# Kernel optimization log

Measured on AMD Instinct MI355X. Metric: run time of the kernel, lower is better.

Reference implementation:

```python
import jax, jax.numpy as jnp
import numpy as np

D = 1024
N_PASSES = 2


def _hadamard(d):
    # Sylvester construction: d must be a power of 2
    H = np.array([[1.0]], dtype=np.float32)
    while H.shape[0] < d:
        H = np.block([[H, H], [H, -H]])
    return H


def setup_inputs() -> dict:
    key = jax.random.key(0)
    kx, ks = jax.random.split(key)
    x = jax.random.normal(kx, (8, 8192, D), dtype=jnp.float32)
    # random +/-1 sign vectors, one per pass
    signs = jnp.where(jax.random.bernoulli(ks, 0.5, (N_PASSES, D)), 1.0, -1.0).astype(jnp.float32)
    h_mat = jnp.asarray(_hadamard(D))  # unnormalized Walsh-Hadamard matrix [D, D]
    return {"x": x, "signs": signs, "h_mat": h_mat}


def reference(x, signs, h_mat):
    # Cascaded SRHT: (sign flip -> WHT -> scale by 1/sqrt(d)) x n_passes
    d = x.shape[-1]
    scale = 1.0 / jnp.sqrt(jnp.asarray(d, dtype=x.dtype))
    out = x
    for i in range(N_PASSES):
        out = (out * signs[i]) @ h_mat * scale
    return out
```

## Files before the change

### kernel.cpp

```cpp
#include <hip/hip_runtime.h>

#define DD 1024

typedef float f32x4 __attribute__((ext_vector_type(4)));

__device__ __forceinline__ void fwht16(float (&v)[16]) {
  #pragma unroll
  for (int h = 1; h < 16; h <<= 1) {
    #pragma unroll
    for (int i = 0; i < 16; ++i) {
      if (!(i & h)) {
        float a = v[i], b = v[i | h];
        v[i]     = a + b;
        v[i | h] = a - b;
      }
    }
  }
}

__device__ __forceinline__ void shfl_stage(float (&v)[16], int mask, int lane) {
  const float sgn = (lane & mask) ? -1.0f : 1.0f;
  #pragma unroll
  for (int j = 0; j < 16; ++j) {
    float o = __shfl_xor(v[j], mask, 64);
    v[j] = fmaf(sgn, v[j], o);
  }
}

__global__ __launch_bounds__(256) void srht_kernel(
    const float* __restrict__ x,
    const float* __restrict__ signs,
    float* __restrict__ out)
{
  __shared__ float lds[4][DD];
  const int lane = threadIdx.x & 63;
  const int wv   = threadIdx.x >> 6;
  const long row = (long)blockIdx.x * 4 + wv;

  const float* __restrict__ xr = x + row * DD;
  float* __restrict__ orow     = out + row * DD;
  const float* __restrict__ s0 = signs;
  const float* __restrict__ s1 = signs + DD;
  float* buf = lds[wv];

  const int lu = lane >> 4;
  const int hb = (lane >> 5) & 1;
  const int m  = (lane >> 2) & 3;
  const int t  = lane & 3;
  const int base_e = 16 * lu + 4 * (m ^ hb) + t;
  const int base_o = 16 * lu + 4 * (m ^ ((hb + 2) & 3)) + t;
  const int qL    = (lane >> 1) & 3;
  const int abase = 16 * lane;

  float s1v[16];
  #pragma unroll
  for (int k = 0; k < 16; ++k) s1v[k] = s1[lane + 64 * k];

  float v[16];

  {
    const f32x4* xp = (const f32x4*)(xr + 16 * lane);
    const f32x4* sp = (const f32x4*)(s0 + 16 * lane);
    #pragma unroll
    for (int c = 0; c < 4; ++c) {
      f32x4 a = xp[c];
      f32x4 s = sp[c];
      v[4 * c + 0] = a.x * s.x;
      v[4 * c + 1] = a.y * s.y;
      v[4 * c + 2] = a.z * s.z;
      v[4 * c + 3] = a.w * s.w;
    }
  }

  fwht16(v);
  shfl_stage(v, 1, lane);
  shfl_stage(v, 2, lane);

  #pragma unroll
  for (int c = 0; c < 4; ++c) {
    f32x4 w4 = {v[4 * c], v[4 * c + 1], v[4 * c + 2], v[4 * c + 3]};
    *(f32x4*)(buf + abase + 4 * (c ^ qL)) = w4;
  }
  #pragma unroll
  for (int k = 0; k < 16; ++k)
    v[k] = buf[((k & 1) ? base_o : base_e) + 64 * k];

  fwht16(v);

  #pragma unroll
  for (int k = 0; k < 16; ++k) v[k] *= s1v[k] * 0.03125f;

  fwht16(v);

  #pragma unroll
  for (int k = 0; k < 16; ++k)
    buf[((k & 1) ? base_o : base_e) + 64 * k] = v[k];
  #pragma unroll
  for (int c = 0; c < 4; ++c) {
    f32x4 r4 = *(const f32x4*)(buf + abase + 4 * (c ^ qL));
    v[4 * c + 0] = r4.x;
    v[4 * c + 1] = r4.y;
    v[4 * c + 2] = r4.z;
    v[4 * c + 3] = r4.w;
  }

  shfl_stage(v, 1, lane);
  shfl_stage(v, 2, lane);
  fwht16(v);

  {
    f32x4* op = (f32x4*)(orow + 16 * lane);
    #pragma unroll
    for (int c = 0; c < 4; ++c) {
      f32x4 r;
      r.x = v[4 * c + 0] * 0.03125f;
      r.y = v[4 * c + 1] * 0.03125f;
      r.z = v[4 * c + 2] * 0.03125f;
      r.w = v[4 * c + 3] * 0.03125f;
      op[c] = r;
    }
  }
}

extern "C" void kernel_launch(void* const* d_in, const int* in_sizes, int n_in,
                              void* d_out, int out_size, void* d_ws, size_t ws_size,
                              hipStream_t stream) {
  const float* x     = (const float*)d_in[0];
  const float* signs = (const float*)d_in[1];
  float* out         = (float*)d_out;

  const int rows   = in_sizes[0] / DD;
  const int blocks = rows / 4;

  hipLaunchKernelGGL(srht_kernel, dim3(blocks), dim3(256), 0, stream,
                     x, signs, out);
}
```

Before: 130.6 us.

## Make SRHT kernel persistent with double-buffered async global-to-LDS row prefetch

The kernel becomes persistent: a fixed grid of 1024 blocks in which each wave loops over rows with a stride. Each wave loads its next row directly into a second LDS slot using global_load_lds, so the read overlaps the butterfly compute on the current row. Explicit vmcnt waits control that overlap. The first sign flip becomes a sign-bit XOR, and the first 1/32 scale is folded into the second sign vector. This aims to hide global memory latency in a bandwidth-bound kernel, at the cost of twice the LDS per wave, lower parallelism, and fragile hand-written waitcnt accounting.

Measured after the change: 124.9 us. -4.4%, faster.

```diff
diff --git a/kernel.cpp b/kernel.cpp
--- a/kernel.cpp
+++ b/kernel.cpp
@@ -1,4 +1,5 @@
 #include <hip/hip_runtime.h>
+#include <stdint.h>
 
 #define DD 1024
 
@@ -27,21 +28,27 @@
   }
 }
 
+__device__ __forceinline__ void dma_row(const float* src_row, float* slot, int lane) {
+  const int swz = 16 * (lane >> 2) + 4 * ((lane & 3) ^ ((lane >> 3) & 3));
+  #pragma unroll
+  for (int c = 0; c < 4; ++c) {
+    __builtin_amdgcn_global_load_lds(
+        (const __attribute__((address_space(1))) void*)(src_row + 256 * c + swz),
+        (__attribute__((address_space(3))) void*)(slot + 256 * c),
+        16, 0, 0);
+  }
+}
+
 __global__ __launch_bounds__(256) void srht_kernel(
     const float* __restrict__ x,
     const float* __restrict__ signs,
-    float* __restrict__ out)
+    float* __restrict__ out,
+    int iters, int wstride)
 {
-  __shared__ float lds[4][DD];
+  __shared__ float lds[4][2][DD];
   const int lane = threadIdx.x & 63;
   const int wv   = threadIdx.x >> 6;
-  const long row = (long)blockIdx.x * 4 + wv;
-
-  const float* __restrict__ xr = x + row * DD;
-  float* __restrict__ orow     = out + row * DD;
-  const float* __restrict__ s0 = signs;
-  const float* __restrict__ s1 = signs + DD;
-  float* buf = lds[wv];
+  const int gw   = blockIdx.x * 4 + wv;
 
   const int lu = lane >> 4;
   const int hb = (lane >> 5) & 1;
@@ -52,73 +59,95 @@
   const int qL    = (lane >> 1) & 3;
   const int abase = 16 * lane;
 
-  float s1v[16];
-  #pragma unroll
-  for (int k = 0; k < 16; ++k) s1v[k] = s1[lane + 64 * k];
-
-  float v[16];
-
+  uint32_t s0m[16];
+  float    s1v[16];
   {
-    const f32x4* xp = (const f32x4*)(xr + 16 * lane);
-    const f32x4* sp = (const f32x4*)(s0 + 16 * lane);
+    const f32x4* sp0 = (const f32x4*)(signs + 16 * lane);
     #pragma unroll
     for (int c = 0; c < 4; ++c) {
-      f32x4 a = xp[c];
-      f32x4 s = sp[c];
-      v[4 * c + 0] = a.x * s.x;
-      v[4 * c + 1] = a.y * s.y;
-      v[4 * c + 2] = a.z * s.z;
-      v[4 * c + 3] = a.w * s.w;
+      f32x4 s = sp0[c];
+      s0m[4 * c + 0] = __float_as_uint(s.x) & 0x80000000u;
+      s0m[4 * c + 1] = __float_as_uint(s.y) & 0x80000000u;
+      s0m[4 * c + 2] = __float_as_uint(s.z) & 0x80000000u;
+      s0m[4 * c + 3] = __float_as_uint(s.w) & 0x80000000u;
     }
+    #pragma unroll
+    for (int k = 0; k < 16; ++k)
+      s1v[k] = signs[DD + lane + 64 * k] * 0.03125f;
   }
 
-  fwht16(v);
-  shfl_stage(v, 1, lane);
-  shfl_stage(v, 2, lane);
+  long r = gw;
+  dma_row(x + r * (long)DD, lds[wv][0], lane);
+  asm volatile("s_waitcnt vmcnt(0)" ::: "memory");
 
-  #pragma unroll
-  for (int c = 0; c < 4; ++c) {
-    f32x4 w4 = {v[4 * c], v[4 * c + 1], v[4 * c + 2], v[4 * c + 3]};
-    *(f32x4*)(buf + abase + 4 * (c ^ qL)) = w4;
-  }
-  #pragma unroll
-  for (int k = 0; k < 16; ++k)
-    v[k] = buf[((k & 1) ? base_o : base_e) + 64 * k];
+  for (int it = 0; it < iters; ++it) {
+    float* slot  = lds[wv][it & 1];
+    float* nslot = lds[wv][(it + 1) & 1];
 
-  fwht16(v);
+    asm volatile("s_waitcnt vmcnt(4)" ::: "memory");
 
-  #pragma unroll
-  for (int k = 0; k < 16; ++k) v[k] *= s1v[k] * 0.03125f;
-
-  fwht16(v);
-
-  #pragma unroll
-  for (int k = 0; k < 16; ++k)
-    buf[((k & 1) ? base_o : base_e) + 64 * k] = v[k];
-  #pragma unroll
-  for (int c = 0; c < 4; ++c) {
-    f32x4 r4 = *(const f32x4*)(buf + abase + 4 * (c ^ qL));
-    v[4 * c + 0] = r4.x;
-    v[4 * c + 1] = r4.y;
-    v[4 * c + 2] = r4.z;
-    v[4 * c + 3] = r4.w;
-  }
-
-  shfl_stage(v, 1, lane);
-  shfl_stage(v, 2, lane);
-  fwht16(v);
-
-  {
-    f32x4* op = (f32x4*)(orow + 16 * lane);
+    float v[16];
     #pragma unroll
     for (int c = 0; c < 4; ++c) {
-      f32x4 r;
-      r.x = v[4 * c + 0] * 0.03125f;
-      r.y = v[4 * c + 1] * 0.03125f;
-      r.z = v[4 * c + 2] * 0.03125f;
-      r.w = v[4 * c + 3] * 0.03125f;
-      op[c] = r;
+      f32x4 a = *(const f32x4*)(slot + abase + 4 * (c ^ qL));
+      v[4 * c + 0] = __uint_as_float(__float_as_uint(a.x) ^ s0m[4 * c + 0]);
+      v[4 * c + 1] = __uint_as_float(__float_as_uint(a.y) ^ s0m[4 * c + 1]);
+      v[4 * c + 2] = __uint_as_float(__float_as_uint(a.z) ^ s0m[4 * c + 2]);
+      v[4 * c + 3] = __uint_as_float(__float_as_uint(a.w) ^ s0m[4 * c + 3]);
     }
+
+    long rn = (it + 1 < iters) ? (r + wstride) : (long)gw;
+    dma_row(x + rn * (long)DD, nslot, lane);
+
+    fwht16(v);
+    shfl_stage(v, 1, lane);
+    shfl_stage(v, 2, lane);
+
+    #pragma unroll
+    for (int c = 0; c < 4; ++c) {
+      f32x4 w4 = {v[4 * c], v[4 * c + 1], v[4 * c + 2], v[4 * c + 3]};
+      *(f32x4*)(slot + abase + 4 * (c ^ qL)) = w4;
+    }
+    #pragma unroll
+    for (int k = 0; k < 16; ++k)
+      v[k] = slot[((k & 1) ? base_o : base_e) + 64 * k];
+
+    fwht16(v);
+
+    #pragma unroll
+    for (int k = 0; k < 16; ++k) v[k] *= s1v[k];
+
+    fwht16(v);
+
+    #pragma unroll
+    for (int k = 0; k < 16; ++k)
+      slot[((k & 1) ? base_o : base_e) + 64 * k] = v[k];
+    #pragma unroll
+    for (int c = 0; c < 4; ++c) {
+      f32x4 r4 = *(const f32x4*)(slot + abase + 4 * (c ^ qL));
+      v[4 * c + 0] = r4.x;
+      v[4 * c + 1] = r4.y;
+      v[4 * c + 2] = r4.z;
+      v[4 * c + 3] = r4.w;
+    }
+
+    shfl_stage(v, 1, lane);
+    shfl_stage(v, 2, lane);
+    fwht16(v);
+
+    {
+      f32x4* op = (f32x4*)(out + r * (long)DD + 16 * lane);
+      #pragma unroll
+      for (int c = 0; c < 4; ++c) {
+        f32x4 o4;
+        o4.x = v[4 * c + 0] * 0.03125f;
+        o4.y = v[4 * c + 1] * 0.03125f;
+        o4.z = v[4 * c + 2] * 0.03125f;
+        o4.w = v[4 * c + 3] * 0.03125f;
+        op[c] = o4;
+      }
+    }
+    r += wstride;
   }
 }
 
@@ -129,9 +158,15 @@
   const float* signs = (const float*)d_in[1];
   float* out         = (float*)d_out;
 
-  const int rows   = in_sizes[0] / DD;
-  const int blocks = rows / 4;
+  const int rows = in_sizes[0] / DD;
+  int blocks = 1024;
+  int waves  = blocks * 4;
+  if (rows % waves != 0) {
+    blocks = rows / 4;
+    waves  = blocks * 4;
+  }
+  const int iters = rows / waves;
 
   hipLaunchKernelGGL(srht_kernel, dim3(blocks), dim3(256), 0, stream,
-                     x, signs, out);
+                     x, signs, out, iters, waves);
 }
```

## Use persistent waves with double-buffered row prefetch and DPP butterfly stages

Applied to the files above, without the earlier changes.

Launches a fixed grid of 2048 blocks, and each wave processes several rows. The next row's load is issued before the current row is computed, so global memory latency overlaps with compute. The cross-lane butterfly stages now use DPP quad permutes instead of __shfl_xor, the first sign flip becomes a bit-XOR from a packed mask, and both scale factors are folded into the second sign vector. This raises register pressure from the extra row buffers and adds a loop with a tail case.

New measurement: 132.1 us. No clear change (+1.1%).

```diff
diff --git a/kernel.cpp b/kernel.cpp
--- a/kernel.cpp
+++ b/kernel.cpp
@@ -1,8 +1,15 @@
 #include <hip/hip_runtime.h>
+#include <stdint.h>
 
 #define DD 1024
 
 typedef float f32x4 __attribute__((ext_vector_type(4)));
+
+template <int CTRL>
+__device__ __forceinline__ float xdpp(float v) {
+  return __int_as_float(__builtin_amdgcn_update_dpp(
+      0, __float_as_int(v), CTRL, 0xF, 0xF, true));
+}
 
 __device__ __forceinline__ void fwht16(float (&v)[16]) {
   #pragma unroll
@@ -18,63 +25,42 @@
   }
 }
 
-__device__ __forceinline__ void shfl_stage(float (&v)[16], int mask, int lane) {
-  const float sgn = (lane & mask) ? -1.0f : 1.0f;
+__device__ __forceinline__ void load_row(const float* __restrict__ x, long r,
+                                         int lane, float (&v)[16]) {
+  const f32x4* p = (const f32x4*)(x + r * (long)DD + 16 * lane);
   #pragma unroll
-  for (int j = 0; j < 16; ++j) {
-    float o = __shfl_xor(v[j], mask, 64);
-    v[j] = fmaf(sgn, v[j], o);
+  for (int c = 0; c < 4; ++c) {
+    f32x4 a = p[c];
+    v[4 * c + 0] = a.x; v[4 * c + 1] = a.y;
+    v[4 * c + 2] = a.z; v[4 * c + 3] = a.w;
   }
 }
 
-__global__ __launch_bounds__(256) void srht_kernel(
-    const float* __restrict__ x,
-    const float* __restrict__ signs,
-    float* __restrict__ out)
+__device__ __forceinline__ void store_row(float* __restrict__ out, long r,
+                                          int lane, const float (&res)[16]) {
+  f32x4* op = (f32x4*)(out + r * (long)DD + 16 * lane);
+  #pragma unroll
+  for (int c = 0; c < 4; ++c) {
+    f32x4 o4 = {res[4 * c + 0], res[4 * c + 1], res[4 * c + 2], res[4 * c + 3]};
+    op[c] = o4;
+  }
+}
+
+__device__ __forceinline__ void process_row(
+    float (&v)[16], float (&res)[16], float* __restrict__ buf,
+    const float (&s1v)[16], uint32_t s0p, float sg1, float sg2,
+    int abase, int qL, int base_e, int base_o)
 {
-  __shared__ float lds[4][DD];
-  const int lane = threadIdx.x & 63;
-  const int wv   = threadIdx.x >> 6;
-  const long row = (long)blockIdx.x * 4 + wv;
-
-  const float* __restrict__ xr = x + row * DD;
-  float* __restrict__ orow     = out + row * DD;
-  const float* __restrict__ s0 = signs;
-  const float* __restrict__ s1 = signs + DD;
-  float* buf = lds[wv];
-
-  const int lu = lane >> 4;
-  const int hb = (lane >> 5) & 1;
-  const int m  = (lane >> 2) & 3;
-  const int t  = lane & 3;
-  const int base_e = 16 * lu + 4 * (m ^ hb) + t;
-  const int base_o = 16 * lu + 4 * (m ^ ((hb + 2) & 3)) + t;
-  const int qL    = (lane >> 1) & 3;
-  const int abase = 16 * lane;
-
-  float s1v[16];
   #pragma unroll
-  for (int k = 0; k < 16; ++k) s1v[k] = s1[lane + 64 * k];
-
-  float v[16];
-
-  {
-    const f32x4* xp = (const f32x4*)(xr + 16 * lane);
-    const f32x4* sp = (const f32x4*)(s0 + 16 * lane);
-    #pragma unroll
-    for (int c = 0; c < 4; ++c) {
-      f32x4 a = xp[c];
-      f32x4 s = sp[c];
-      v[4 * c + 0] = a.x * s.x;
-      v[4 * c + 1] = a.y * s.y;
-      v[4 * c + 2] = a.z * s.z;
-      v[4 * c + 3] = a.w * s.w;
-    }
-  }
+  for (int j = 0; j < 16; ++j)
+    v[j] = __uint_as_float(__float_as_uint(v[j]) ^
+                           ((s0p << (31 - j)) & 0x80000000u));
 
   fwht16(v);
-  shfl_stage(v, 1, lane);
-  shfl_stage(v, 2, lane);
+  #pragma unroll
+  for (int j = 0; j < 16; ++j) { float o = xdpp<0xB1>(v[j]); v[j] = fmaf(sg1, v[j], o); }
+  #pragma unroll
+  for (int j = 0; j < 16; ++j) { float o = xdpp<0x4E>(v[j]); v[j] = fmaf(sg2, v[j], o); }
 
   #pragma unroll
   for (int c = 0; c < 4; ++c) {
@@ -88,7 +74,7 @@
   fwht16(v);
 
   #pragma unroll
-  for (int k = 0; k < 16; ++k) v[k] *= s1v[k] * 0.03125f;
+  for (int k = 0; k < 16; ++k) v[k] *= s1v[k];
 
   fwht16(v);
 
@@ -98,27 +84,79 @@
   #pragma unroll
   for (int c = 0; c < 4; ++c) {
     f32x4 r4 = *(const f32x4*)(buf + abase + 4 * (c ^ qL));
-    v[4 * c + 0] = r4.x;
-    v[4 * c + 1] = r4.y;
-    v[4 * c + 2] = r4.z;
-    v[4 * c + 3] = r4.w;
+    res[4 * c + 0] = r4.x; res[4 * c + 1] = r4.y;
+    res[4 * c + 2] = r4.z; res[4 * c + 3] = r4.w;
   }
 
-  shfl_stage(v, 1, lane);
-  shfl_stage(v, 2, lane);
-  fwht16(v);
+  #pragma unroll
+  for (int j = 0; j < 16; ++j) { float o = xdpp<0xB1>(res[j]); res[j] = fmaf(sg1, res[j], o); }
+  #pragma unroll
+  for (int j = 0; j < 16; ++j) { float o = xdpp<0x4E>(res[j]); res[j] = fmaf(sg2, res[j], o); }
+  fwht16(res);
+}
 
+__global__ __launch_bounds__(256) void srht_kernel(
+    const float* __restrict__ x, const float* __restrict__ signs,
+    float* __restrict__ out, int iters, int NW, int rows)
+{
+  __shared__ float lds[4][DD];
+  const int lane = threadIdx.x & 63;
+  const int wv   = threadIdx.x >> 6;
+  const int gw   = blockIdx.x * 4 + wv;
+  if (gw >= rows) return;
+  float* buf = lds[wv];
+
+  const int qL    = (lane >> 1) & 3;
+  const int abase = 16 * lane;
+  const int lu = lane >> 4;
+  const int hb = (lane >> 5) & 1;
+  const int m  = (lane >> 2) & 3;
+  const int t  = lane & 3;
+  const int base_e = 16 * lu + 4 * (m ^ hb) + t;
+  const int base_o = 16 * lu + 4 * (m ^ ((hb + 2) & 3)) + t;
+
+  const float sg1 = (lane & 1) ? -1.f : 1.f;
+  const float sg2 = (lane & 2) ? -1.f : 1.f;
+
+  uint32_t s0p = 0;
   {
-    f32x4* op = (f32x4*)(orow + 16 * lane);
+    const f32x4* sp0 = (const f32x4*)(signs + 16 * lane);
     #pragma unroll
     for (int c = 0; c < 4; ++c) {
-      f32x4 r;
-      r.x = v[4 * c + 0] * 0.03125f;
-      r.y = v[4 * c + 1] * 0.03125f;
-      r.z = v[4 * c + 2] * 0.03125f;
-      r.w = v[4 * c + 3] * 0.03125f;
-      op[c] = r;
+      f32x4 a = sp0[c];
+      s0p |= (__float_as_uint(a.x) >> 31) << (4 * c + 0);
+      s0p |= (__float_as_uint(a.y) >> 31) << (4 * c + 1);
+      s0p |= (__float_as_uint(a.z) >> 31) << (4 * c + 2);
+      s0p |= (__float_as_uint(a.w) >> 31) << (4 * c + 3);
     }
+  }
+  float s1v[16];
+  #pragma unroll
+  for (int k = 0; k < 16; ++k)
+    s1v[k] = signs[DD + lane + 64 * k] * (1.0f / 1024.0f);
+
+  float vA[16], vB[16], res[16];
+  long rA = gw;
+  long rB = gw + (long)NW;
+  load_row(x, rA, lane, vA);
+  if (iters > 1) load_row(x, rB, lane, vB);
+
+  for (int it = 0; it + 1 < iters; it += 2) {
+    process_row(vA, res, buf, s1v, s0p, sg1, sg2, abase, qL, base_e, base_o);
+    store_row(out, rA, lane, res);
+    long rnA = rA + 2L * NW;
+    if (it + 2 < iters && rnA < rows) load_row(x, rnA, lane, vA);
+
+    process_row(vB, res, buf, s1v, s0p, sg1, sg2, abase, qL, base_e, base_o);
+    store_row(out, rB, lane, res);
+    long rnB = rB + 2L * NW;
+    if (it + 3 < iters && rnB < rows) load_row(x, rnB, lane, vB);
+
+    rA = rnA; rB = rnB;
+  }
+  if (iters & 1) {
+    process_row(vA, res, buf, s1v, s0p, sg1, sg2, abase, qL, base_e, base_o);
+    store_row(out, rA, lane, res);
   }
 }
 
@@ -129,9 +167,12 @@
   const float* signs = (const float*)d_in[1];
   float* out         = (float*)d_out;
 
-  const int rows   = in_sizes[0] / DD;
-  const int blocks = rows / 4;
+  const int rows = in_sizes[0] / DD;
+  int blocks = 2048;
+  if (rows < blocks * 4) blocks = (rows + 3) / 4;
+  const int NW    = blocks * 4;
+  const int iters = (rows + NW - 1) / NW;
 
   hipLaunchKernelGGL(srht_kernel, dim3(blocks), dim3(256), 0, stream,
-                     x, signs, out);
+                     x, signs, out, iters, NW, rows);
 }
```
